# Performance work log

Measured on AMD Instinct MI355X. Metric: run time of the kernel, lower is better.

Reference implementation:

```python
import jax, jax.numpy as jnp
from jax import lax
import numpy as np

STRIDES = (2, 2)
PADDING = 'SAME'
EPS = 1e-05


def setup_inputs() -> dict:
    key = jax.random.key(0)
    k1, k2, k3 = jax.random.split(key, 3)
    x = jax.random.normal(k1, (16, 64, 64, 256), dtype=jnp.float32)
    # flax default conv kernel init ~ lecun_normal; plain normal scaled is fine for a math reference
    kernel = jax.random.normal(k2, (4, 4, 256, 128), dtype=jnp.float32) * 0.05
    bias = jax.random.normal(k3, (128,), dtype=jnp.float32) * 0.01
    alpha = jnp.ones((1,), dtype=jnp.float32)
    return {'x': x, 'kernel': kernel, 'bias': bias, 'alpha': alpha}


def reference(x, kernel, bias, alpha):
    # x: [B, H, W, Cin] NHWC; kernel: [kh, kw, Cin, Cout]
    out_features = kernel.shape[-1]

    # main transposed conv: dot-product map  [B, H*2, W*2, Cout]
    dot = lax.conv_transpose(x, kernel, STRIDES, PADDING, transpose_kernel=False)

    # patch squared-sum map: conv_transpose of x**2 with an all-ones kernel
    # of shape kernel_size + (Cin, 1); broadcast over Cout (same math as jnp.repeat)
    ones_k = jnp.ones(kernel.shape[:-1] + (1,), dtype=kernel.dtype)
    patch_sq = lax.conv_transpose(x * x, ones_k, STRIDES, PADDING, transpose_kernel=False)  # [B, H', W', 1]

    # per-filter kernel squared norm, reduced over (kh, kw, Cin) -> [Cout]
    k_sq = jnp.sum(kernel * kernel, axis=(0, 1, 2))

    # ||x_patch - W||^2 = sum(x^2) + sum(W^2) - 2 * <x, W>
    dist_sq = patch_sq + k_sq - 2.0 * dot

    y = (dot * dot) / (dist_sq + EPS)
    y = y + bias  # broadcast over [B, H', W', Cout]

    nf = jnp.float32(out_features)
    scale = (jnp.sqrt(nf) / jnp.log1p(nf)) ** alpha  # alpha shape (1,) broadcasts
    return y * scale
```

## Files before the change

### kernel.cpp

```cpp
#include <hip/hip_runtime.h>
#include <cstdint>
#include <cstddef>

#define CIN   256
#define COUT  128

typedef float  f32x4  __attribute__((ext_vector_type(4)));
typedef __bf16 bf16x8 __attribute__((ext_vector_type(8)));
typedef unsigned int u32x4 __attribute__((ext_vector_type(4)));

#define XPAD_BYTES (16ull*66*66*256*2)
#define WT_OFF     XPAD_BYTES
#define WT_BYTES   (16ull*128*256*2)
#define SPAD_OFF   (WT_OFF + WT_BYTES)
#define SPAD_BYTES (16ull*66*66*4)
#define KSQ_OFF    (SPAD_OFF + SPAD_BYTES)
#define WS_NEEDED  (KSQ_OFF + 512)

__device__ __forceinline__ unsigned short f2bf(float f) {
  unsigned int u = __float_as_uint(f);
  u += 0x7fffu + ((u >> 16) & 1u);
  return (unsigned short)(u >> 16);
}

__device__ __forceinline__ void async16(const void* lds, const void* g) {
  __builtin_amdgcn_global_load_lds(
      (const __attribute__((address_space(1))) unsigned int*)g,
      (__attribute__((address_space(3))) unsigned int*)lds, 16, 0, 0);
}

__global__ __launch_bounds__(256) void prep_all(
    const float* __restrict__ x, const float* __restrict__ w,
    unsigned short* __restrict__ xpad, unsigned short* __restrict__ wt,
    float* __restrict__ spad, float* __restrict__ ksq)
{
  __shared__ __align__(16) unsigned short lw[32*128];
  __shared__ float red[256];
  int blk = blockIdx.x;
  int t = threadIdx.x;

  if (blk < 17424) {
    int wave = t >> 6, lane = t & 63;
    int p = blk * 4 + wave;
    int b = p / 4356;
    int rem = p - b * 4356;
    int iyp = rem / 66, ixp = rem - iyp * 66;
    bool interior = (iyp >= 1 && iyp <= 64 && ixp >= 1 && ixp <= 64);
    f32x4 v = {0.f, 0.f, 0.f, 0.f};
    if (interior) {
      const float* src = x + (((size_t)b*64 + (iyp-1))*64 + (ixp-1))*CIN + lane*4;
      v = *(const f32x4*)src;
    }
    ushort4 h;
    h.x = f2bf(v.x); h.y = f2bf(v.y); h.z = f2bf(v.z); h.w = f2bf(v.w);
    *(ushort4*)(xpad + (size_t)p*CIN + lane*4) = h;
    float s = v.x*v.x + v.y*v.y + v.z*v.z + v.w*v.w;
    #pragma unroll
    for (int off = 32; off > 0; off >>= 1) s += __shfl_down(s, off);
    if (lane == 0) spad[p] = s;
  } else if (blk < 17552) {
    int pblk = blk - 17424;
    int tap = pblk >> 3;
    int ci0 = (pblk & 7) * 32;
    int co4 = (t & 31) * 4;
    #pragma unroll
    for (int i = 0; i < 4; ++i) {
      int ci = (t >> 5) + i*8;
      const float* src = w + ((size_t)(tap*256 + ci0 + ci))*COUT + co4;
      f32x4 v = *(const f32x4*)src;
      ushort4 h; h.x = f2bf(v.x); h.y = f2bf(v.y); h.z = f2bf(v.z); h.w = f2bf(v.w);
      *(ushort4*)&lw[ci*128 + co4] = h;
    }
    __syncthreads();
    int co = t >> 1, h16 = (t & 1) * 16;
    union { unsigned short u[16]; uint4 q[2]; } tmp;
    #pragma unroll
    for (int i = 0; i < 16; ++i) tmp.u[i] = lw[(h16 + i)*128 + co];
    uint4* dst = (uint4*)(wt + ((size_t)tap*128 + co)*CIN + ci0 + h16);
    dst[0] = tmp.q[0]; dst[1] = tmp.q[1];
  } else {
    int co = blk - 17552;
    float s = 0.f;
    for (int j = t; j < 4096; j += 256) { float v = w[(size_t)j*COUT + co]; s += v*v; }
    red[t] = s; __syncthreads();
    for (int off = 128; off > 0; off >>= 1) {
      if (t < off) red[t] += red[t + off];
      __syncthreads();
    }
    if (t == 0) ksq[co] = red[0];
  }
}

__global__ __launch_bounds__(256, 3) void yat_main(
    const unsigned short* __restrict__ xpad,
    const unsigned short* __restrict__ wt,
    const float* __restrict__ spad,
    const float* __restrict__ ksq,
    const float* __restrict__ bias,
    const float* __restrict__ alpha,
    float* __restrict__ out)
{
  __shared__ __align__(16) unsigned short xsA[2][6656];
  __shared__ __align__(16) unsigned short xsB[3][4096];
  __shared__ float srow[198];

  int orig = blockIdx.x;
  int bid = (orig & 7) * 256 + (orig >> 3);
  int px = bid & 1, py = (bid >> 1) & 1, u2 = (bid >> 2) & 31, b = bid >> 7;
  int t = threadIdx.x, wave = t >> 6, lane = t & 63;
  int rp = wave >> 1, coh = wave & 1;
  int l15 = lane & 15, l4 = lane >> 4;
  int bRow0 = 2*u2 + py;

  if (t < 198) {
    int r = t / 66, c = t - r*66;
    srow[t] = spad[((size_t)b*66 + bRow0 + r)*66 + c];
  }
  asm volatile("s_waitcnt vmcnt(0) lgkmcnt(0)" ::: "memory");

  const char* srcA[4];
  unsigned short* dstA[4];
  {
    #pragma unroll
    for (int r = 0; r < 3; ++r) {
      int seg = r*256 + t;
      int row = seg / 264; int r2 = seg - row*264;
      int col = r2 >> 2, q = r2 & 3;
      srcA[r] = (const char*)xpad
              + (((size_t)(b*66 + bRow0 + row))*66 + col)*512
              + ((q ^ ((col>>1)&3))*16);
      dstA[r] = &xsA[0][0] + (size_t)(r*2048 + wave*512);
    }
    int l = t & 63;
    int seg = 768 + ((l < 24) ? l : 23);
    int row = seg / 264; int r2 = seg - row*264;
    int col = r2 >> 2, q = r2 & 3;
    srcA[3] = (const char*)xpad
            + (((size_t)(b*66 + bRow0 + row))*66 + col)*512
            + ((q ^ ((col>>1)&3))*16);
    dstA[3] = &xsA[0][0] + 6144;
  }
  const char* srcB[2];
  unsigned short* dstB[2];
  {
    int baseTap = py*4 + px;
    #pragma unroll
    for (int r = 0; r < 2; ++r) {
      int seg = r*256 + t;
      int co = seg >> 2, qd = seg & 3;
      srcB[r] = (const char*)wt + (size_t)baseTap*65536
              + (size_t)co*512 + ((qd ^ ((co>>1)&3))*16);
      dstB[r] = &xsB[0][0] + (size_t)(r*2048 + wave*512);
    }
  }

  unsigned abA[2];
  #pragma unroll
  for (int bb = 0; bb < 2; ++bb) {
    int c0 = l15 + px + bb;
    abA[bb] = (unsigned)(size_t)(&xsA[0][0])
            + (unsigned)(rp*4224 + c0*64 + ((l4 ^ ((c0>>1)&3)) << 4));
  }
  unsigned abB = (unsigned)(size_t)(&xsB[0][0])
               + (unsigned)((coh*64 + l15)*64 + ((l4 ^ ((l15>>1)&3)) << 4));

  f32x4 acc[4][4];
  #pragma unroll
  for (int i = 0; i < 4; ++i)
    #pragma unroll
    for (int j = 0; j < 4; ++j)
      acc[i][j] = (f32x4){0.f, 0.f, 0.f, 0.f};

  u32x4 Af[4], Bf[4];

#define SB  __builtin_amdgcn_sched_barrier(0)
#define BAR __builtin_amdgcn_s_barrier()
#define VMW(N) do { asm volatile("s_waitcnt vmcnt(" #N ")" ::: "memory"); SB; } while (0)
#define LGK(N) do { asm volatile("s_waitcnt lgkmcnt(" #N ")" ::: "memory"); SB; } while (0)
#define DSR(dst, addr, off)                                                \
  asm volatile("ds_read_b128 %0, %1 offset:%c2"                            \
               : "=v"(dst) : "v"(addr), "i"(off))

#define STG_B(BI2, OFF) {                                                  \
    async16(dstB[0] + (size_t)(BI2)*4096, srcB[0] + (OFF));                \
    async16(dstB[1] + (size_t)(BI2)*4096, srcB[1] + (OFF)); }
#define STG_A(BUF2, OFF) {                                                 \
    async16(dstA[0] + (size_t)(BUF2)*6656, srcA[0] + (OFF));               \
    async16(dstA[1] + (size_t)(BUF2)*6656, srcA[1] + (OFF));               \
    async16(dstA[2] + (size_t)(BUF2)*6656, srcA[2] + (OFF));               \
    async16(dstA[3] + (size_t)(BUF2)*6656, srcA[3] + (OFF)); }

#define MFMA16 {                                                           \
    _Pragma("unroll")                                                      \
    for (int mt = 0; mt < 4; ++mt)                                         \
      _Pragma("unroll")                                                    \
      for (int nt = 0; nt < 4; ++nt)                                       \
        acc[mt][nt] = __builtin_amdgcn_mfma_f32_16x16x32_bf16(             \
            __builtin_bit_cast(bf16x8, Af[mt]),                            \
            __builtin_bit_cast(bf16x8, Bf[nt]),                            \
            acc[mt][nt], 0, 0, 0); }

#define CH(N, BUFA, AA, BB, BI, DOB, BI2, OFFB, DOA, BUFA2, OFFA) {        \
    VMW(N); BAR;                                                           \
    DSR(Af[0], abA[BB], (BUFA)*13312 + (AA)*4224 + 0);                     \
    DSR(Af[1], abA[BB], (BUFA)*13312 + (AA)*4224 + 1024);                  \
    DSR(Af[2], abA[BB], (BUFA)*13312 + (AA)*4224 + 2048);                  \
    DSR(Af[3], abA[BB], (BUFA)*13312 + (AA)*4224 + 3072);                  \
    DSR(Bf[0], abB, (BI)*8192 + 0);                                        \
    DSR(Bf[1], abB, (BI)*8192 + 1024);                                     \
    DSR(Bf[2], abB, (BI)*8192 + 2048);                                     \
    DSR(Bf[3], abB, (BI)*8192 + 3072);                                     \
    SB;                                                                    \
    if (DOB) STG_B(BI2, OFFB);                                             \
    if (DOA) STG_A(BUFA2, OFFA);                                           \
    SB;                                                                    \
    LGK(0);                                                                \
    __builtin_amdgcn_s_setprio(1); MFMA16;                                 \
    __builtin_amdgcn_s_setprio(0); SB; }

  SB;
  STG_B(0, 0);
  STG_A(0, 0);
  STG_B(1, 131072);
  SB;

  CH(2, 0,0,0, 0,  1, 2, 524288,                1, 1, 64);
  CH(6, 0,0,1, 1,  1, 0, 524288+131072,         0, 0, 0);
  CH(6, 0,1,0, 2,  1, 1, 64,                    0, 0, 0);
  CH(2, 0,1,1, 0,  1, 2, 131072+64,             0, 0, 0);
  CH(2, 1,0,0, 1,  1, 0, 524288+64,             1, 0, 128);
  CH(6, 1,0,1, 2,  1, 1, 524288+131072+64,      0, 0, 0);
  CH(6, 1,1,0, 0,  1, 2, 128,                   0, 0, 0);
  CH(2, 1,1,1, 1,  1, 0, 131072+128,            0, 0, 0);
  CH(2, 0,0,0, 2,  1, 1, 524288+128,            1, 1, 192);
  CH(6, 0,0,1, 0,  1, 2, 524288+131072+128,     0, 0, 0);
  CH(6, 0,1,0, 1,  1, 0, 192,                   0, 0, 0);
  CH(2, 0,1,1, 2,  1, 1, 131072+192,            0, 0, 0);
  CH(2, 1,0,0, 0,  1, 2, 524288+192,            1, 0, 256);
  CH(6, 1,0,1, 1,  1, 0, 524288+131072+192,     0, 0, 0);
  CH(6, 1,1,0, 2,  1, 1, 256,                   0, 0, 0);
  CH(2, 1,1,1, 0,  1, 2, 131072+256,            0, 0, 0);
  CH(2, 0,0,0, 1,  1, 0, 524288+256,            1, 1, 320);
  CH(6, 0,0,1, 2,  1, 1, 524288+131072+256,     0, 0, 0);
  CH(6, 0,1,0, 0,  1, 2, 320,                   0, 0, 0);
  CH(2, 0,1,1, 1,  1, 0, 131072+320,            0, 0, 0);
  CH(2, 1,0,0, 2,  1, 1, 524288+320,            1, 0, 384);
  CH(6, 1,0,1, 0,  1, 2, 524288+131072+320,     0, 0, 0);
  CH(6, 1,1,0, 1,  1, 0, 384,                   0, 0, 0);
  CH(2, 1,1,1, 2,  1, 1, 131072+384,            0, 0, 0);
  CH(2, 0,0,0, 0,  1, 2, 524288+384,            1, 1, 448);
  CH(6, 0,0,1, 1,  1, 0, 524288+131072+384,     0, 0, 0);
  CH(6, 0,1,0, 2,  1, 1, 448,                   0, 0, 0);
  CH(2, 0,1,1, 0,  1, 2, 131072+448,            0, 0, 0);
  CH(2, 1,0,0, 1,  1, 0, 524288+448,            0, 0, 0);
  CH(2, 1,0,1, 2,  1, 1, 524288+131072+448,     0, 0, 0);
  CH(2, 1,1,0, 0,  0, 0, 0,                     0, 0, 0);
  CH(0, 1,1,1, 1,  0, 0, 0,                     0, 0, 0);

#undef SB
#undef BAR
#undef VMW
#undef LGK
#undef DSR
#undef STG_B
#undef STG_A
#undef MFMA16
#undef CH

  float scale = powf(sqrtf(128.f) / log1pf(128.f), alpha[0]);
  float kq[4], bi[4];
  #pragma unroll
  for (int nt = 0; nt < 4; ++nt) {
    int n = coh*64 + nt*16 + l15;
    kq[nt] = ksq[n]; bi[nt] = bias[n];
  }
  int oy = 2*(2*u2 + rp) + py;
  size_t orow = ((size_t)b*128 + oy) * 128 * COUT;
  #pragma unroll
  for (int mt = 0; mt < 4; ++mt) {
    #pragma unroll
    for (int r = 0; r < 4; ++r) {
      int v = mt*16 + l4*4 + r;
      int vpx = v + px;
      float ps = srow[rp*66 + vpx] + srow[rp*66 + vpx + 1]
               + srow[rp*66 + 66 + vpx] + srow[rp*66 + 66 + vpx + 1];
      #pragma unroll
      for (int nt = 0; nt < 4; ++nt) {
        float dot = acc[mt][nt][r];
        float dist = ps + kq[nt] - 2.f*dot + 1e-5f;
        float y = (dot*dot/dist + bi[nt]) * scale;
        int n = coh*64 + nt*16 + l15;
        out[orow + (size_t)(2*v + px)*COUT + n] = y;
      }
    }
  }
}

__global__ __launch_bounds__(256) void fb_ksq(const float* __restrict__ w,
                                              float* __restrict__ ksq) {
  __shared__ float red[256];
  int co = blockIdx.x, t = threadIdx.x;
  float s = 0.f;
  for (int j = t; j < 4096; j += 256) { float v = w[(size_t)j*COUT + co]; s += v*v; }
  red[t] = s; __syncthreads();
  for (int off = 128; off > 0; off >>= 1) {
    if (t < off) red[t] += red[t + off];
    __syncthreads();
  }
  if (t == 0) ksq[co] = red[0];
}

__global__ __launch_bounds__(256) void fb_main(
    const float* __restrict__ x, const float* __restrict__ w,
    const float* __restrict__ bias, const float* __restrict__ alpha,
    const float* __restrict__ ksq, float* __restrict__ out)
{
  size_t idx = (size_t)blockIdx.x * 256 + threadIdx.x;
  int co = (int)(idx & 127);
  int ox = (int)((idx >> 7) & 127);
  int oy = (int)((idx >> 14) & 127);
  int b  = (int)(idx >> 21);
  int py = oy & 1, px = ox & 1, u = oy >> 1, v = ox >> 1;
  float dot = 0.f, ps = 0.f;
  for (int a = 0; a < 2; ++a) {
    int iy = u + py + a - 1;
    if (iy < 0 || iy > 63) continue;
    for (int b2 = 0; b2 < 2; ++b2) {
      int ix = v + px + b2 - 1;
      if (ix < 0 || ix > 63) continue;
      const float* xp = x + (((size_t)b*64 + iy)*64 + ix)*CIN;
      const float* wp = w + ((size_t)((py + 2*a)*4 + (px + 2*b2))*CIN)*COUT + co;
      for (int ci = 0; ci < CIN; ++ci) {
        float xv = xp[ci];
        dot += xv * wp[(size_t)ci*COUT];
        ps  += xv * xv;
      }
    }
  }
  float dist = ps + ksq[co] - 2.f*dot + 1e-5f;
  float scale = powf(sqrtf(128.f) / log1pf(128.f), alpha[0]);
  out[idx] = (dot*dot/dist + bias[co]) * scale;
}

extern "C" void kernel_launch(void* const* d_in, const int* in_sizes, int n_in,
                              void* d_out, int out_size, void* d_ws, size_t ws_size,
                              hipStream_t stream)
{
  const float* x     = (const float*)d_in[0];
  const float* w     = (const float*)d_in[1];
  const float* bias  = (const float*)d_in[2];
  const float* alpha = (const float*)d_in[3];
  float* out = (float*)d_out;

  if (ws_size < WS_NEEDED) {
    float* ksq = (float*)d_ws;
    fb_ksq<<<128, 256, 0, stream>>>(w, ksq);
    fb_main<<<131072, 256, 0, stream>>>(x, w, bias, alpha, ksq, out);
    return;
  }

  unsigned short* xpad = (unsigned short*)d_ws;
  unsigned short* wtp  = (unsigned short*)((char*)d_ws + WT_OFF);
  float* spad = (float*)((char*)d_ws + SPAD_OFF);
  float* ksq  = (float*)((char*)d_ws + KSQ_OFF);

  prep_all<<<17680, 256, 0, stream>>>(x, w, xpad, wtp, spad, ksq);
  yat_main<<<2048, 256, 0, stream>>>(xpad, wtp, spad, ksq, bias, alpha, out);
}
```

Baseline: 103.0 us.

## Enlarge block tile to four output rows by full Cout per wave

Each block now covers four input-row pairs instead of two, and each wave computes all 128 output channels for one row instead of half. This halves the grid and doubles the per-wave accumulator tile, so each B fragment read from LDS is reused across more rows and less staging traffic is needed per output. The A staging buffer grows to hold five rows (with a scrap target for spare lanes), occupancy drops to two blocks per CU, and the MFMA loop is split into two halves behind partial LDS waits. The risks are higher register pressure and fewer resident waves available to hide latency.

After: 97.75 us. 1.05x faster.

```diff
diff --git a/kernel.cpp b/kernel.cpp
--- a/kernel.cpp
+++ b/kernel.cpp
@@ -91,7 +91,7 @@
   }
 }
 
-__global__ __launch_bounds__(256, 3) void yat_main(
+__global__ __launch_bounds__(256, 2) void yat_main(
     const unsigned short* __restrict__ xpad,
     const unsigned short* __restrict__ wt,
     const float* __restrict__ spad,
@@ -100,29 +100,31 @@
     const float* __restrict__ alpha,
     float* __restrict__ out)
 {
-  __shared__ __align__(16) unsigned short xsA[2][6656];
+  __shared__ __align__(16) unsigned short xsA[2][11264];
   __shared__ __align__(16) unsigned short xsB[3][4096];
-  __shared__ float srow[198];
+  __shared__ __align__(16) unsigned short scrap[512];
+  __shared__ float srow[330];
 
   int orig = blockIdx.x;
-  int bid = (orig & 7) * 256 + (orig >> 3);
-  int px = bid & 1, py = (bid >> 1) & 1, u2 = (bid >> 2) & 31, b = bid >> 7;
+  int bid = (orig & 7) * 128 + (orig >> 3);
+  int px = bid & 1, py = (bid >> 1) & 1, u4 = (bid >> 2) & 15, b = bid >> 6;
   int t = threadIdx.x, wave = t >> 6, lane = t & 63;
-  int rp = wave >> 1, coh = wave & 1;
+  int rp = wave;
   int l15 = lane & 15, l4 = lane >> 4;
-  int bRow0 = 2*u2 + py;
-
-  if (t < 198) {
-    int r = t / 66, c = t - r*66;
-    srow[t] = spad[((size_t)b*66 + bRow0 + r)*66 + c];
+  int bRow0 = u4*4 + py;
+
+  for (int i = t; i < 330; i += 256) {
+    int r = i / 66, c = i - r*66;
+    srow[i] = spad[((size_t)b*66 + bRow0 + r)*66 + c];
   }
   asm volatile("s_waitcnt vmcnt(0) lgkmcnt(0)" ::: "memory");
 
-  const char* srcA[4];
-  unsigned short* dstA[4];
+  const char* srcA[6];
+  unsigned short* dstA[6];
+  int mulA[6];
   {
     #pragma unroll
-    for (int r = 0; r < 3; ++r) {
+    for (int r = 0; r < 5; ++r) {
       int seg = r*256 + t;
       int row = seg / 264; int r2 = seg - row*264;
       int col = r2 >> 2, q = r2 & 3;
@@ -130,15 +132,16 @@
               + (((size_t)(b*66 + bRow0 + row))*66 + col)*512
               + ((q ^ ((col>>1)&3))*16);
       dstA[r] = &xsA[0][0] + (size_t)(r*2048 + wave*512);
-    }
-    int l = t & 63;
-    int seg = 768 + ((l < 24) ? l : 23);
+      mulA[r] = 11264;
+    }
+    int seg = 1280 + t; if (seg > 1319) seg = 1319;
     int row = seg / 264; int r2 = seg - row*264;
     int col = r2 >> 2, q = r2 & 3;
-    srcA[3] = (const char*)xpad
+    srcA[5] = (const char*)xpad
             + (((size_t)(b*66 + bRow0 + row))*66 + col)*512
             + ((q ^ ((col>>1)&3))*16);
-    dstA[3] = &xsA[0][0] + 6144;
+    dstA[5] = (wave == 0) ? (&xsA[0][0] + 10240) : &scrap[0];
+    mulA[5] = (wave == 0) ? 11264 : 0;
   }
   const char* srcB[2];
   unsigned short* dstB[2];
@@ -162,16 +165,16 @@
             + (unsigned)(rp*4224 + c0*64 + ((l4 ^ ((c0>>1)&3)) << 4));
   }
   unsigned abB = (unsigned)(size_t)(&xsB[0][0])
-               + (unsigned)((coh*64 + l15)*64 + ((l4 ^ ((l15>>1)&3)) << 4));
-
-  f32x4 acc[4][4];
+               + (unsigned)(l15*64 + ((l4 ^ ((l15>>1)&3)) << 4));
+
+  f32x4 acc[4][8];
   #pragma unroll
   for (int i = 0; i < 4; ++i)
     #pragma unroll
-    for (int j = 0; j < 4; ++j)
+    for (int j = 0; j < 8; ++j)
       acc[i][j] = (f32x4){0.f, 0.f, 0.f, 0.f};
 
-  u32x4 Af[4], Bf[4];
+  u32x4 Af[4], Bf[8];
 
 #define SB  __builtin_amdgcn_sched_barrier(0)
 #define BAR __builtin_amdgcn_s_barrier()
@@ -185,16 +188,18 @@
     async16(dstB[0] + (size_t)(BI2)*4096, srcB[0] + (OFF));                \
     async16(dstB[1] + (size_t)(BI2)*4096, srcB[1] + (OFF)); }
 #define STG_A(BUF2, OFF) {                                                 \
-    async16(dstA[0] + (size_t)(BUF2)*6656, srcA[0] + (OFF));               \
-    async16(dstA[1] + (size_t)(BUF2)*6656, srcA[1] + (OFF));               \
-    async16(dstA[2] + (size_t)(BUF2)*6656, srcA[2] + (OFF));               \
-    async16(dstA[3] + (size_t)(BUF2)*6656, srcA[3] + (OFF)); }
-
-#define MFMA16 {                                                           \
+    async16(dstA[0] + (size_t)(BUF2)*mulA[0], srcA[0] + (OFF));            \
+    async16(dstA[1] + (size_t)(BUF2)*mulA[1], srcA[1] + (OFF));            \
+    async16(dstA[2] + (size_t)(BUF2)*mulA[2], srcA[2] + (OFF));            \
+    async16(dstA[3] + (size_t)(BUF2)*mulA[3], srcA[3] + (OFF));            \
+    async16(dstA[4] + (size_t)(BUF2)*mulA[4], srcA[4] + (OFF));            \
+    async16(dstA[5] + (size_t)(BUF2)*mulA[5], srcA[5] + (OFF)); }
+
+#define MFMA_H(NT0) {                                                      \
     _Pragma("unroll")                                                      \
     for (int mt = 0; mt < 4; ++mt)                                         \
       _Pragma("unroll")                                                    \
-      for (int nt = 0; nt < 4; ++nt)                                       \
+      for (int nt = NT0; nt < NT0 + 4; ++nt)                               \
         acc[mt][nt] = __builtin_amdgcn_mfma_f32_16x16x32_bf16(             \
             __builtin_bit_cast(bf16x8, Af[mt]),                            \
             __builtin_bit_cast(bf16x8, Bf[nt]),                            \
@@ -202,21 +207,26 @@
 
 #define CH(N, BUFA, AA, BB, BI, DOB, BI2, OFFB, DOA, BUFA2, OFFA) {        \
     VMW(N); BAR;                                                           \
-    DSR(Af[0], abA[BB], (BUFA)*13312 + (AA)*4224 + 0);                     \
-    DSR(Af[1], abA[BB], (BUFA)*13312 + (AA)*4224 + 1024);                  \
-    DSR(Af[2], abA[BB], (BUFA)*13312 + (AA)*4224 + 2048);                  \
-    DSR(Af[3], abA[BB], (BUFA)*13312 + (AA)*4224 + 3072);                  \
+    DSR(Af[0], abA[BB], (BUFA)*22528 + (AA)*4224 + 0);                     \
+    DSR(Af[1], abA[BB], (BUFA)*22528 + (AA)*4224 + 1024);                  \
+    DSR(Af[2], abA[BB], (BUFA)*22528 + (AA)*4224 + 2048);                  \
+    DSR(Af[3], abA[BB], (BUFA)*22528 + (AA)*4224 + 3072);                  \
     DSR(Bf[0], abB, (BI)*8192 + 0);                                        \
     DSR(Bf[1], abB, (BI)*8192 + 1024);                                     \
     DSR(Bf[2], abB, (BI)*8192 + 2048);                                     \
     DSR(Bf[3], abB, (BI)*8192 + 3072);                                     \
+    DSR(Bf[4], abB, (BI)*8192 + 4096);                                     \
+    DSR(Bf[5], abB, (BI)*8192 + 5120);                                     \
+    DSR(Bf[6], abB, (BI)*8192 + 6144);                                     \
+    DSR(Bf[7], abB, (BI)*8192 + 7168);                                     \
     SB;                                                                    \
     if (DOB) STG_B(BI2, OFFB);                                             \
     if (DOA) STG_A(BUFA2, OFFA);                                           \
     SB;                                                                    \
+    LGK(4);                                                                \
+    __builtin_amdgcn_s_setprio(1); MFMA_H(0);                              \
     LGK(0);                                                                \
-    __builtin_amdgcn_s_setprio(1); MFMA16;                                 \
-    __builtin_amdgcn_s_setprio(0); SB; }
+    MFMA_H(4); __builtin_amdgcn_s_setprio(0); SB; }
 
   SB;
   STG_B(0, 0);
@@ -225,32 +235,32 @@
   SB;
 
   CH(2, 0,0,0, 0,  1, 2, 524288,                1, 1, 64);
-  CH(6, 0,0,1, 1,  1, 0, 524288+131072,         0, 0, 0);
-  CH(6, 0,1,0, 2,  1, 1, 64,                    0, 0, 0);
+  CH(8, 0,0,1, 1,  1, 0, 524288+131072,         0, 0, 0);
+  CH(8, 0,1,0, 2,  1, 1, 64,                    0, 0, 0);
   CH(2, 0,1,1, 0,  1, 2, 131072+64,             0, 0, 0);
   CH(2, 1,0,0, 1,  1, 0, 524288+64,             1, 0, 128);
-  CH(6, 1,0,1, 2,  1, 1, 524288+131072+64,      0, 0, 0);
-  CH(6, 1,1,0, 0,  1, 2, 128,                   0, 0, 0);
+  CH(8, 1,0,1, 2,  1, 1, 524288+131072+64,      0, 0, 0);
+  CH(8, 1,1,0, 0,  1, 2, 128,                   0, 0, 0);
   CH(2, 1,1,1, 1,  1, 0, 131072+128,            0, 0, 0);
   CH(2, 0,0,0, 2,  1, 1, 524288+128,            1, 1, 192);
-  CH(6, 0,0,1, 0,  1, 2, 524288+131072+128,     0, 0, 0);
-  CH(6, 0,1,0, 1,  1, 0, 192,                   0, 0, 0);
+  CH(8, 0,0,1, 0,  1, 2, 524288+131072+128,     0, 0, 0);
+  CH(8, 0,1,0, 1,  1, 0, 192,                   0, 0, 0);
   CH(2, 0,1,1, 2,  1, 1, 131072+192,            0, 0, 0);
   CH(2, 1,0,0, 0,  1, 2, 524288+192,            1, 0, 256);
-  CH(6, 1,0,1, 1,  1, 0, 524288+131072+192,     0, 0, 0);
-  CH(6, 1,1,0, 2,  1, 1, 256,                   0, 0, 0);
+  CH(8, 1,0,1, 1,  1, 0, 524288+131072+192,     0, 0, 0);
+  CH(8, 1,1,0, 2,  1, 1, 256,                   0, 0, 0);
   CH(2, 1,1,1, 0,  1, 2, 131072+256,            0, 0, 0);
   CH(2, 0,0,0, 1,  1, 0, 524288+256,            1, 1, 320);
-  CH(6, 0,0,1, 2,  1, 1, 524288+131072+256,     0, 0, 0);
-  CH(6, 0,1,0, 0,  1, 2, 320,                   0, 0, 0);
+  CH(8, 0,0,1, 2,  1, 1, 524288+131072+256,     0, 0, 0);
+  CH(8, 0,1,0, 0,  1, 2, 320,                   0, 0, 0);
   CH(2, 0,1,1, 1,  1, 0, 131072+320,            0, 0, 0);
   CH(2, 1,0,0, 2,  1, 1, 524288+320,            1, 0, 384);
-  CH(6, 1,0,1, 0,  1, 2, 524288+131072+320,     0, 0, 0);
-  CH(6, 1,1,0, 1,  1, 0, 384,                   0, 0, 0);
+  CH(8, 1,0,1, 0,  1, 2, 524288+131072+320,     0, 0, 0);
+  CH(8, 1,1,0, 1,  1, 0, 384,                   0, 0, 0);
   CH(2, 1,1,1, 2,  1, 1, 131072+384,            0, 0, 0);
   CH(2, 0,0,0, 0,  1, 2, 524288+384,            1, 1, 448);
-  CH(6, 0,0,1, 1,  1, 0, 524288+131072+384,     0, 0, 0);
-  CH(6, 0,1,0, 2,  1, 1, 448,                   0, 0, 0);
+  CH(8, 0,0,1, 1,  1, 0, 524288+131072+384,     0, 0, 0);
+  CH(8, 0,1,0, 2,  1, 1, 448,                   0, 0, 0);
   CH(2, 0,1,1, 0,  1, 2, 131072+448,            0, 0, 0);
   CH(2, 1,0,0, 1,  1, 0, 524288+448,            0, 0, 0);
   CH(2, 1,0,1, 2,  1, 1, 524288+131072+448,     0, 0, 0);
@@ -264,17 +274,17 @@
 #undef DSR
 #undef STG_B
 #undef STG_A
-#undef MFMA16
+#undef MFMA_H
 #undef CH
 
   float scale = powf(sqrtf(128.f) / log1pf(128.f), alpha[0]);
-  float kq[4], bi[4];
+  float kq[8], bi[8];
   #pragma unroll
-  for (int nt = 0; nt < 4; ++nt) {
-    int n = coh*64 + nt*16 + l15;
+  for (int nt = 0; nt < 8; ++nt) {
+    int n = nt*16 + l15;
     kq[nt] = ksq[n]; bi[nt] = bias[n];
   }
-  int oy = 2*(2*u2 + rp) + py;
+  int oy = 2*(u4*4 + rp) + py;
   size_t orow = ((size_t)b*128 + oy) * 128 * COUT;
   #pragma unroll
   for (int mt = 0; mt < 4; ++mt) {
@@ -285,11 +295,11 @@
       float ps = srow[rp*66 + vpx] + srow[rp*66 + vpx + 1]
                + srow[rp*66 + 66 + vpx] + srow[rp*66 + 66 + vpx + 1];
       #pragma unroll
-      for (int nt = 0; nt < 4; ++nt) {
+      for (int nt = 0; nt < 8; ++nt) {
         float dot = acc[mt][nt][r];
         float dist = ps + kq[nt] - 2.f*dot + 1e-5f;
         float y = (dot*dot/dist + bi[nt]) * scale;
-        int n = coh*64 + nt*16 + l15;
+        int n = nt*16 + l15;
         out[orow + (size_t)(2*v + px)*COUT + n] = y;
       }
     }
@@ -365,5 +375,5 @@
   float* ksq  = (float*)((char*)d_ws + KSQ_OFF);
 
   prep_all<<<17680, 256, 0, stream>>>(x, w, xpad, wtp, spad, ksq);
-  yat_main<<<2048, 256, 0, stream>>>(xpad, wtp, spad, ksq, bias, alpha, out);
-}
+  yat_main<<<1024, 256, 0, stream>>>(xpad, wtp, spad, ksq, bias, alpha, out);
+}
```
